# Kernel optimization log

Hardware: AMD Instinct MI355X
Metric: run time of the kernel (lower is better)

Reference implementation:

```python
import jax, jax.numpy as jnp
import numpy as np

B, S, D, DK, DV = 4, 4096, 1024, 64, 64


def setup_inputs() -> dict:
    rng = jax.random.key(0)
    k1, k2, k3, k4, k5, k6 = jax.random.split(rng, 6)
    query = jax.random.normal(k1, (B, S, D), dtype=jnp.float32)
    key = jax.random.normal(k2, (B, S, D), dtype=jnp.float32)
    value = jax.random.normal(k3, (B, S, D), dtype=jnp.float32)
    Wq = jax.random.normal(k4, (D, DK), dtype=jnp.float32)
    Wk = jax.random.normal(k5, (D, DK), dtype=jnp.float32)
    Wv = jax.random.normal(k6, (D, DV), dtype=jnp.float32)
    mask = jnp.tril(jnp.ones((S, S), dtype=jnp.bool_))  # causal mask, broadcasts over batch
    return {"query": query, "key": key, "value": value,
            "Wq": Wq, "Wk": Wk, "Wv": Wv, "mask": mask}


def reference(query, key, value, Wq, Wk, Wv, mask):
    # linear projections: [B,S,D] @ [D,dk] -> [B,S,dk]
    q = jnp.matmul(query, Wq)
    k = jnp.matmul(key, Wk)
    v = jnp.matmul(value, Wv)
    scale = 1.0 / jnp.sqrt(jnp.asarray(DK, dtype=q.dtype))
    # scores: [B,S,S]
    attn = jnp.einsum("bqd,bkd->bqk", q, k) * scale
    attn = jnp.where(mask, attn, -jnp.inf)  # mask==0 -> -inf
    attn = jax.nn.softmax(attn, axis=-1)
    x = jnp.matmul(attn, v)  # [B,S,dv]
    return x
```

## Files before the change

kernel.cpp:

```cpp
#include <hip/hip_runtime.h>
#include <math.h>


#define SEQ 4096
#define DIM 1024
#define HD  64
#define NB  4
#define NSPLIT 4

typedef __attribute__((ext_vector_type(4))) float    f32x4;
typedef __attribute__((ext_vector_type(8))) _Float16 f16x8;
typedef __attribute__((ext_vector_type(4))) _Float16 f16x4;

#define MFMA16 __builtin_amdgcn_mfma_f32_16x16x32_f16

#define GLD16(dst, ptr, imm)                                        \
  asm volatile("global_load_dwordx4 %0, %1, off offset:" #imm      \
               : "=&v"(dst) : "v"(ptr))

#define VMWAIT(n)                                                   \
  do {                                                              \
    asm volatile("s_waitcnt vmcnt(" #n ")" ::: "memory");           \
    __builtin_amdgcn_sched_barrier(0);                              \
  } while (0)

#define LGKMBAR()                                                   \
  do {                                                              \
    asm volatile("s_waitcnt lgkmcnt(0)" ::: "memory");              \
    __builtin_amdgcn_sched_barrier(0);                              \
    asm volatile("s_barrier" ::: "memory");                         \
    __builtin_amdgcn_sched_barrier(0);                              \
  } while (0)

__device__ __forceinline__ int SW(int row, int k) {
  return row * 64 + (k ^ ((row & 7) << 3));
}

__global__ __launch_bounds__(256) void wsplit_kernel(
    const float* __restrict__ Wq, const float* __restrict__ Wk,
    const float* __restrict__ Wv, _Float16* __restrict__ wf)
{
  const int which = blockIdx.x;
  const int kt    = blockIdx.y;
  const float* __restrict__ W = (which == 0) ? Wq : (which == 1) ? Wk : Wv;
  const float scale = (which == 0) ? 0.18033688011112042f : 1.0f;
  const size_t tb = ((size_t)which * 16 + kt) * 8192;
#pragma unroll
  for (int i = 0; i < 2; ++i) {
    const int pair = threadIdx.x + 256 * i;
    const int lane = pair & 63, f = pair >> 6;
    const int ks = f >> 2, ct = f & 3;
    const int col = ct * 16 + (lane & 15);
    const int k0 = kt * 64 + ks * 32 + (lane >> 4) * 8;
    f16x8 hv, lv;
#pragma unroll
    for (int j = 0; j < 8; ++j) {
      const float y = W[(size_t)(k0 + j) * HD + col] * scale;
      const _Float16 h = (_Float16)y;
      hv[j] = h;
      lv[j] = (_Float16)(y - (float)h);
    }
    *(f16x8*)&wf[tb + (size_t)f * 512 + lane * 8]       = hv;
    *(f16x8*)&wf[tb + (size_t)(8 + f) * 512 + lane * 8] = lv;
  }
}

__global__ __launch_bounds__(256, 2) void proj_kernel(
    const float* __restrict__ Xq, const float* __restrict__ Xk,
    const float* __restrict__ Xv,
    const _Float16* __restrict__ wf,
    _Float16* __restrict__ qh, _Float16* __restrict__ ql,
    _Float16* __restrict__ kh, _Float16* __restrict__ kl,
    _Float16* __restrict__ vt)
{
  __shared__ __attribute__((aligned(16))) float    Xs[2][64 * 64];
  __shared__ __attribute__((aligned(16))) _Float16 Ws[2][8192];

  const int which = blockIdx.y;
  const float* __restrict__ X = (which == 0) ? Xq : (which == 1) ? Xk : Xv;

  const int t = threadIdx.x, lane = t & 63, w = t >> 6;
  const int bm = blockIdx.x * 64;

  const float* gX[4];
  int xdst[4];
#pragma unroll
  for (int i = 0; i < 4; ++i) {
    const int row = w * 16 + i * 4 + (lane >> 4);
    gX[i] = X + (size_t)(bm + row) * DIM + (lane & 15) * 4;
    xdst[i] = row * 64 + (((lane & 15) ^ (row & 15)) * 4);
  }
  const _Float16* gW0 = wf + (size_t)which * 131072 + (w * 4) * 512 + lane * 8;
  int wdst[4];
#pragma unroll
  for (int i = 0; i < 4; ++i) wdst[i] = (w * 4 + i) * 512 + lane * 8;

  const int frow = lane & 15;
  const int ldsrow = w * 16 + frow;

  f32x4 acc[4] = {{0,0,0,0},{0,0,0,0},{0,0,0,0},{0,0,0,0}};
  f32x4 xA[4], xB[4];
  f16x8 wA[4], wB[4];

#define LOADT(xs, ws, kt)                                            \
  do {                                                               \
    const float* xb0 = gX[0] + (kt) * 64;                            \
    const float* xb1 = gX[1] + (kt) * 64;                            \
    const float* xb2 = gX[2] + (kt) * 64;                            \
    const float* xb3 = gX[3] + (kt) * 64;                            \
    GLD16(xs[0], xb0, 0);                                            \
    GLD16(xs[1], xb1, 0);                                            \
    GLD16(xs[2], xb2, 0);                                            \
    GLD16(xs[3], xb3, 0);                                            \
    const _Float16* wb = gW0 + (size_t)(kt) * 8192;                  \
    GLD16(ws[0], wb, 0);                                             \
    GLD16(ws[1], wb, 1024);                                          \
    GLD16(ws[2], wb, 2048);                                          \
    GLD16(ws[3], wb, 3072);                                          \
  } while (0)

#define WRITET(xs, ws, buf)                                          \
  do {                                                               \
    _Pragma("unroll")                                                \
    for (int i = 0; i < 4; ++i) *(f32x4*)&Xs[buf][xdst[i]] = xs[i];  \
    _Pragma("unroll")                                                \
    for (int i = 0; i < 4; ++i) *(f16x8*)&Ws[buf][wdst[i]] = ws[i];  \
  } while (0)

#define COMPUTET(buf)                                                     \
  do {                                                                    \
    _Pragma("unroll")                                                     \
    for (int ks = 0; ks < 2; ++ks) {                                      \
      const int cc0 = ks * 8 + (lane >> 4) * 2;                           \
      f32x4 x0 = *(const f32x4*)&Xs[buf][ldsrow * 64 + ((cc0 ^ frow) * 4)];       \
      f32x4 x1 = *(const f32x4*)&Xs[buf][ldsrow * 64 + (((cc0 + 1) ^ frow) * 4)]; \
      f16x8 xh, xl;                                                       \
      _Pragma("unroll")                                                   \
      for (int j = 0; j < 4; ++j) {                                       \
        const _Float16 h0 = (_Float16)x0[j];                              \
        xh[j] = h0; xl[j] = (_Float16)(x0[j] - (float)h0);                \
        const _Float16 h1 = (_Float16)x1[j];                              \
        xh[j + 4] = h1; xl[j + 4] = (_Float16)(x1[j] - (float)h1);        \
      }                                                                   \
      _Pragma("unroll")                                                   \
      for (int ct = 0; ct < 4; ++ct) {                                    \
        f16x8 bh = *(const f16x8*)&Ws[buf][(ks * 4 + ct) * 512 + lane * 8];       \
        f16x8 bl = *(const f16x8*)&Ws[buf][(8 + ks * 4 + ct) * 512 + lane * 8];   \
        acc[ct] = MFMA16(xh, bh, acc[ct], 0, 0, 0);                       \
        acc[ct] = MFMA16(xl, bh, acc[ct], 0, 0, 0);                       \
        acc[ct] = MFMA16(xh, bl, acc[ct], 0, 0, 0);                       \
      }                                                                   \
    }                                                                     \
  } while (0)

  LOADT(xA, wA, 0);
  LOADT(xB, wB, 1);

#pragma unroll 1
  for (int kt = 0; kt < 12; kt += 2) {
    VMWAIT(8);
    WRITET(xA, wA, 0);
    LOADT(xA, wA, kt + 2);
    LGKMBAR();
    COMPUTET(0);
    VMWAIT(8);
    WRITET(xB, wB, 1);
    LOADT(xB, wB, kt + 3);
    LGKMBAR();
    COMPUTET(1);
  }
  VMWAIT(8);  WRITET(xA, wA, 0);  LOADT(xA, wA, 14);  LGKMBAR();  COMPUTET(0);
  VMWAIT(8);  WRITET(xB, wB, 1);  LOADT(xB, wB, 15);  LGKMBAR();  COMPUTET(1);
  VMWAIT(8);  WRITET(xA, wA, 0);                      LGKMBAR();  COMPUTET(0);
  VMWAIT(0);  WRITET(xB, wB, 1);                      LGKMBAR();  COMPUTET(1);
#undef LOADT
#undef WRITET
#undef COMPUTET

  const size_t orow0 = (size_t)bm + w * 16 + (lane >> 4) * 4;
  if (which < 2) {
    _Float16* oh = (which == 0) ? qh : kh;
    _Float16* ol = (which == 0) ? ql : kl;
#pragma unroll
    for (int ct = 0; ct < 4; ++ct)
#pragma unroll
      for (int r = 0; r < 4; ++r) {
        const float y = acc[ct][r];
        const _Float16 h = (_Float16)y;
        const size_t idx = (orow0 + r) * HD + ct * 16 + (lane & 15);
        oh[idx] = h;
        ol[idx] = (_Float16)(y - (float)h);
      }
  } else {
    const int batch = (int)(orow0 >> 12);
    const int pos = (int)(orow0 & 4095);
#pragma unroll
    for (int ct = 0; ct < 4; ++ct) {
      f16x4 hv;
#pragma unroll
      for (int r = 0; r < 4; ++r) hv[r] = (_Float16)acc[ct][r];
      *(f16x4*)&vt[((size_t)batch * HD + ct * 16 + (lane & 15)) * SEQ + pos] = hv;
    }
  }
}

__global__ __launch_bounds__(256) void attn_kernel(
    const _Float16* __restrict__ qh, const _Float16* __restrict__ ql,
    const _Float16* __restrict__ kh, const _Float16* __restrict__ kl,
    const _Float16* __restrict__ vt,
    _Float16* __restrict__ opart, float* __restrict__ mlp)
{
  __shared__ __attribute__((aligned(16))) _Float16 Ksh[64 * 64];
  __shared__ __attribute__((aligned(16))) _Float16 Ksl[64 * 64];
  __shared__ __attribute__((aligned(16))) _Float16 Vs [64 * 64];
  __shared__ __attribute__((aligned(16))) _Float16 Pt [64 * 64];

  const int t = threadIdx.x, lane = t & 63, w = t >> 6;
  const int b = blockIdx.y;
  const int p = blockIdx.x >> 2, s = blockIdx.x & 3;
  const size_t bS = (size_t)b * SEQ;

  for (int sel = 0; sel < 2; ++sel) {
    const int qb = sel ? (63 - p) : p;
    const int qrow0 = qb * 64 + w * 16;
    const int nt = (qb >= s) ? ((qb - s) >> 2) + 1 : 0;

    float m[4] = {-INFINITY, -INFINITY, -INFINITY, -INFINITY};
    float lsum[4] = {0.f, 0.f, 0.f, 0.f};
    f32x4 o[4] = {{0,0,0,0},{0,0,0,0},{0,0,0,0},{0,0,0,0}};

    if (nt > 0) {
      const _Float16* qhp = qh + (bS + qrow0 + (lane & 15)) * HD + ((lane >> 4) * 8);
      const _Float16* qlp = ql + (bS + qrow0 + (lane & 15)) * HD + ((lane >> 4) * 8);
      f16x8 qhf[2], qlf[2];
      qhf[0] = *(const f16x8*)(qhp);      qhf[1] = *(const f16x8*)(qhp + 32);
      qlf[0] = *(const f16x8*)(qlp);      qlf[1] = *(const f16x8*)(qlp + 32);

      for (int i = 0; i < nt; ++i) {
        const int kt = s + 4 * i;
        const int j0 = kt * 64;

        __syncthreads();
#pragma unroll
        for (int c = 0; c < 2; ++c) {
          const int lin = t + 256 * c;
          const int row = lin >> 3, d8 = (lin & 7) * 8;
          const int dst = SW(row, d8);
          *(f16x8*)&Ksh[dst] = *(const f16x8*)&kh[(bS + j0 + row) * HD + d8];
          *(f16x8*)&Ksl[dst] = *(const f16x8*)&kl[(bS + j0 + row) * HD + d8];
          *(f16x8*)&Vs[dst]  = *(const f16x8*)&vt[((size_t)b * HD + row) * SEQ + j0 + d8];
        }
        __syncthreads();

        f32x4 sacc[4] = {{0,0,0,0},{0,0,0,0},{0,0,0,0},{0,0,0,0}};
#pragma unroll
        for (int kk = 0; kk < 2; ++kk)
#pragma unroll
          for (int kt4 = 0; kt4 < 4; ++kt4) {
            const int ba = SW(kt4 * 16 + (lane & 15), kk * 32 + (lane >> 4) * 8);
            f16x8 bh = *(const f16x8*)&Ksh[ba];
            f16x8 bl = *(const f16x8*)&Ksl[ba];
            sacc[kt4] = MFMA16(qhf[kk], bh, sacc[kt4], 0, 0, 0);
            sacc[kt4] = MFMA16(qlf[kk], bh, sacc[kt4], 0, 0, 0);
            sacc[kt4] = MFMA16(qhf[kk], bl, sacc[kt4], 0, 0, 0);
          }

        if (kt == qb) {
#pragma unroll
          for (int kt4 = 0; kt4 < 4; ++kt4) {
            const int key = j0 + kt4 * 16 + (lane & 15);
#pragma unroll
            for (int r = 0; r < 4; ++r)
              if (key > qrow0 + (lane >> 4) * 4 + r) sacc[kt4][r] = -INFINITY;
          }
        }

        float alf[4];
#pragma unroll
        for (int r = 0; r < 4; ++r) {
          float mx = fmaxf(fmaxf(sacc[0][r], sacc[1][r]),
                           fmaxf(sacc[2][r], sacc[3][r]));
          mx = fmaxf(mx, __shfl_xor(mx, 1));
          mx = fmaxf(mx, __shfl_xor(mx, 2));
          mx = fmaxf(mx, __shfl_xor(mx, 4));
          mx = fmaxf(mx, __shfl_xor(mx, 8));
          const float mn = fmaxf(m[r], mx);
          const float al = exp2f(m[r] - mn);
          const int prow = w * 16 + (lane >> 4) * 4 + r;
          float ps = 0.f;
#pragma unroll
          for (int kt4 = 0; kt4 < 4; ++kt4) {
            const _Float16 ph = (_Float16)exp2f(sacc[kt4][r] - mn);
            ps += (float)ph;
            Pt[SW(prow, kt4 * 16 + (lane & 15))] = ph;
          }
          ps += __shfl_xor(ps, 1);
          ps += __shfl_xor(ps, 2);
          ps += __shfl_xor(ps, 4);
          ps += __shfl_xor(ps, 8);
          lsum[r] = lsum[r] * al + ps;
          m[r] = mn;
          alf[r] = al;
        }
        const f32x4 av = {alf[0], alf[1], alf[2], alf[3]};
#pragma unroll
        for (int ct = 0; ct < 4; ++ct) o[ct] *= av;

#pragma unroll
        for (int kk = 0; kk < 2; ++kk) {
          f16x8 pa = *(const f16x8*)&Pt[SW(w * 16 + (lane & 15),
                                           kk * 32 + (lane >> 4) * 8)];
#pragma unroll
          for (int ct = 0; ct < 4; ++ct) {
            f16x8 vb = *(const f16x8*)&Vs[SW(ct * 16 + (lane & 15),
                                             kk * 32 + (lane >> 4) * 8)];
            o[ct] = MFMA16(pa, vb, o[ct], 0, 0, 0);
          }
        }
      }
    }

    f32x4 invv;
#pragma unroll
    for (int r = 0; r < 4; ++r) invv[r] = (nt > 0) ? 1.0f / lsum[r] : 0.0f;
    const size_t ridx0 = (size_t)(b * NSPLIT + s) * SEQ + qrow0 + (lane >> 4) * 4;
#pragma unroll
    for (int ct = 0; ct < 4; ++ct)
#pragma unroll
      for (int r = 0; r < 4; ++r)
        opart[(ridx0 + r) * HD + ct * 16 + (lane & 15)] =
            (_Float16)(o[ct][r] * invv[r]);
    if ((lane & 15) == 0) {
#pragma unroll
      for (int r = 0; r < 4; ++r) {
        mlp[(ridx0 + r) * 2]     = m[r];
        mlp[(ridx0 + r) * 2 + 1] = lsum[r];
      }
    }
  }
}

__global__ __launch_bounds__(256) void combine_kernel(
    const _Float16* __restrict__ opart, const float* __restrict__ mlp,
    float* __restrict__ out)
{
  const int g = blockIdx.x * 256 + threadIdx.x;
  const int row = g >> 4;
  const int cq = (g & 15) * 4;
  const int b = row >> 12, pos = row & 4095;

  float mv[4], lv[4], msx = -INFINITY;
#pragma unroll
  for (int s = 0; s < 4; ++s) {
    const size_t ri = (size_t)(b * NSPLIT + s) * SEQ + pos;
    mv[s] = mlp[ri * 2];
    lv[s] = mlp[ri * 2 + 1];
    msx = fmaxf(msx, mv[s]);
  }
  f32x4 num = {0.f, 0.f, 0.f, 0.f};
  float L = 0.f;
#pragma unroll
  for (int s = 0; s < 4; ++s) {
    const float wgt = lv[s] * exp2f(mv[s] - msx);
    L += wgt;
    const size_t ri = (size_t)(b * NSPLIT + s) * SEQ + pos;
    const f16x4 ov = *(const f16x4*)&opart[ri * HD + cq];
#pragma unroll
    for (int j = 0; j < 4; ++j) num[j] += wgt * (float)ov[j];
  }
  const float inv = 1.0f / L;
  f32x4 res = {num[0] * inv, num[1] * inv, num[2] * inv, num[3] * inv};
  *(f32x4*)&out[(size_t)row * HD + cq] = res;
}

extern "C" void kernel_launch(void* const* d_in, const int* in_sizes, int n_in,
                              void* d_out, int out_size, void* d_ws, size_t ws_size,
                              hipStream_t stream) {
  const float* query = (const float*)d_in[0];
  const float* key   = (const float*)d_in[1];
  const float* value = (const float*)d_in[2];
  const float* Wq    = (const float*)d_in[3];
  const float* Wk    = (const float*)d_in[4];
  const float* Wv    = (const float*)d_in[5];

  float* out = (float*)d_out;

  _Float16* qh  = (_Float16*)d_ws;
  _Float16* ql  = qh  + (size_t)NB * SEQ * HD;
  _Float16* kh  = ql  + (size_t)NB * SEQ * HD;
  _Float16* kl  = kh  + (size_t)NB * SEQ * HD;
  _Float16* vt  = kl  + (size_t)NB * SEQ * HD;
  _Float16* wf  = vt  + (size_t)NB * SEQ * HD;
  _Float16* opart = wf + (size_t)3 * 16 * 8192;
  float* mlp = (float*)(opart + (size_t)NB * NSPLIT * SEQ * HD);

  wsplit_kernel<<<dim3(3, 16), 256, 0, stream>>>(Wq, Wk, Wv, wf);
  proj_kernel<<<dim3(256, 3), 256, 0, stream>>>(query, key, value, wf,
                                                qh, ql, kh, kl, vt);
  attn_kernel<<<dim3(128, NB), 256, 0, stream>>>(qh, ql, kh, kl, vt, opart, mlp);
  combine_kernel<<<1024, 256, 0, stream>>>(opart, mlp, out);
}
```

Before: 94.61 us.

## Load X operand directly into registers, skipping LDS staging in projection kernel

The projection kernel no longer stages the fp32 X tile through shared memory. Each lane now loads the X fragments it needs for MFMA straight from global memory into registers, in batches of four k-tiles, while only the W tiles still go through LDS. This removes the LDS writes and reads for X, the swizzle bookkeeping and half of the shared memory, which may allow more occupancy. The cost is less overlap: the old loop prefetched the next tile while computing the current one, and the new loop waits on each batch of loads with no cross-iteration prefetch. It also holds more registers live, and global accesses per lane become strided rows.

```diff
diff --git a/kernel.cpp b/kernel.cpp
--- a/kernel.cpp
+++ b/kernel.cpp
@@ -73,7 +73,6 @@
     _Float16* __restrict__ kh, _Float16* __restrict__ kl,
     _Float16* __restrict__ vt)
 {
-  __shared__ __attribute__((aligned(16))) float    Xs[2][64 * 64];
   __shared__ __attribute__((aligned(16))) _Float16 Ws[2][8192];
 
   const int which = blockIdx.y;
@@ -82,58 +81,29 @@
   const int t = threadIdx.x, lane = t & 63, w = t >> 6;
   const int bm = blockIdx.x * 64;
 
-  const float* gX[4];
-  int xdst[4];
-#pragma unroll
-  for (int i = 0; i < 4; ++i) {
-    const int row = w * 16 + i * 4 + (lane >> 4);
-    gX[i] = X + (size_t)(bm + row) * DIM + (lane & 15) * 4;
-    xdst[i] = row * 64 + (((lane & 15) ^ (row & 15)) * 4);
-  }
+  const float* xb = X + (size_t)(bm + w * 16 + (lane & 15)) * DIM
+                      + ((lane >> 4) * 8);
   const _Float16* gW0 = wf + (size_t)which * 131072 + (w * 4) * 512 + lane * 8;
   int wdst[4];
 #pragma unroll
   for (int i = 0; i < 4; ++i) wdst[i] = (w * 4 + i) * 512 + lane * 8;
 
-  const int frow = lane & 15;
-  const int ldsrow = w * 16 + frow;
-
   f32x4 acc[4] = {{0,0,0,0},{0,0,0,0},{0,0,0,0},{0,0,0,0}};
-  f32x4 xA[4], xB[4];
-  f16x8 wA[4], wB[4];
-
-#define LOADT(xs, ws, kt)                                            \
-  do {                                                               \
-    const float* xb0 = gX[0] + (kt) * 64;                            \
-    const float* xb1 = gX[1] + (kt) * 64;                            \
-    const float* xb2 = gX[2] + (kt) * 64;                            \
-    const float* xb3 = gX[3] + (kt) * 64;                            \
-    GLD16(xs[0], xb0, 0);                                            \
-    GLD16(xs[1], xb1, 0);                                            \
-    GLD16(xs[2], xb2, 0);                                            \
-    GLD16(xs[3], xb3, 0);                                            \
-    const _Float16* wb = gW0 + (size_t)(kt) * 8192;                  \
-    GLD16(ws[0], wb, 0);                                             \
-    GLD16(ws[1], wb, 1024);                                          \
-    GLD16(ws[2], wb, 2048);                                          \
-    GLD16(ws[3], wb, 3072);                                          \
-  } while (0)
-
-#define WRITET(xs, ws, buf)                                          \
+  f32x4 xr[16];
+  f16x8 wrA[4], wrB[4], wrC[4], wrD[4];
+
+#define WWRITE(wr, buf)                                              \
   do {                                                               \
     _Pragma("unroll")                                                \
-    for (int i = 0; i < 4; ++i) *(f32x4*)&Xs[buf][xdst[i]] = xs[i];  \
-    _Pragma("unroll")                                                \
-    for (int i = 0; i < 4; ++i) *(f16x8*)&Ws[buf][wdst[i]] = ws[i];  \
+    for (int i = 0; i < 4; ++i) *(f16x8*)&Ws[buf][wdst[i]] = wr[i];  \
   } while (0)
 
-#define COMPUTET(buf)                                                     \
+#define COMPT(buf, base)                                                  \
   do {                                                                    \
     _Pragma("unroll")                                                     \
     for (int ks = 0; ks < 2; ++ks) {                                      \
-      const int cc0 = ks * 8 + (lane >> 4) * 2;                           \
-      f32x4 x0 = *(const f32x4*)&Xs[buf][ldsrow * 64 + ((cc0 ^ frow) * 4)];       \
-      f32x4 x1 = *(const f32x4*)&Xs[buf][ldsrow * 64 + (((cc0 + 1) ^ frow) * 4)]; \
+      f32x4 x0 = xr[(base) + 2 * ks];                                     \
+      f32x4 x1 = xr[(base) + 2 * ks + 1];                                 \
       f16x8 xh, xl;                                                       \
       _Pragma("unroll")                                                   \
       for (int j = 0; j < 4; ++j) {                                       \
@@ -153,29 +123,41 @@
     }                                                                     \
   } while (0)
 
-  LOADT(xA, wA, 0);
-  LOADT(xB, wB, 1);
-
 #pragma unroll 1
-  for (int kt = 0; kt < 12; kt += 2) {
+  for (int ss = 0; ss < 4; ++ss) {
+    const float* xs = xb + ss * 256;
+    GLD16(xr[0],  xs, 0);    GLD16(xr[1],  xs, 16);
+    GLD16(xr[2],  xs, 128);  GLD16(xr[3],  xs, 144);
+    GLD16(xr[4],  xs, 256);  GLD16(xr[5],  xs, 272);
+    GLD16(xr[6],  xs, 384);  GLD16(xr[7],  xs, 400);
+    GLD16(xr[8],  xs, 512);  GLD16(xr[9],  xs, 528);
+    GLD16(xr[10], xs, 640);  GLD16(xr[11], xs, 656);
+    GLD16(xr[12], xs, 768);  GLD16(xr[13], xs, 784);
+    GLD16(xr[14], xs, 896);  GLD16(xr[15], xs, 912);
+    const _Float16* wt0 = gW0 + (size_t)(4 * ss) * 8192;
+    const _Float16* wt1 = wt0 + 8192;
+    const _Float16* wt2 = wt0 + 16384;
+    const _Float16* wt3 = wt0 + 24576;
+    GLD16(wrA[0], wt0, 0); GLD16(wrA[1], wt0, 1024);
+    GLD16(wrA[2], wt0, 2048); GLD16(wrA[3], wt0, 3072);
+    GLD16(wrB[0], wt1, 0); GLD16(wrB[1], wt1, 1024);
+    GLD16(wrB[2], wt1, 2048); GLD16(wrB[3], wt1, 3072);
+    GLD16(wrC[0], wt2, 0); GLD16(wrC[1], wt2, 1024);
+    GLD16(wrC[2], wt2, 2048); GLD16(wrC[3], wt2, 3072);
+    GLD16(wrD[0], wt3, 0); GLD16(wrD[1], wt3, 1024);
+    GLD16(wrD[2], wt3, 2048); GLD16(wrD[3], wt3, 3072);
+
+    VMWAIT(12);
+    WWRITE(wrA, 0);  LGKMBAR();  COMPT(0, 0);
     VMWAIT(8);
-    WRITET(xA, wA, 0);
-    LOADT(xA, wA, kt + 2);
-    LGKMBAR();
-    COMPUTET(0);
-    VMWAIT(8);
-    WRITET(xB, wB, 1);
-    LOADT(xB, wB, kt + 3);
-    LGKMBAR();
-    COMPUTET(1);
-  }
-  VMWAIT(8);  WRITET(xA, wA, 0);  LOADT(xA, wA, 14);  LGKMBAR();  COMPUTET(0);
-  VMWAIT(8);  WRITET(xB, wB, 1);  LOADT(xB, wB, 15);  LGKMBAR();  COMPUTET(1);
-  VMWAIT(8);  WRITET(xA, wA, 0);                      LGKMBAR();  COMPUTET(0);
-  VMWAIT(0);  WRITET(xB, wB, 1);                      LGKMBAR();  COMPUTET(1);
-#undef LOADT
-#undef WRITET
-#undef COMPUTET
+    WWRITE(wrB, 1);  LGKMBAR();  COMPT(1, 4);
+    VMWAIT(4);
+    WWRITE(wrC, 0);  LGKMBAR();  COMPT(0, 8);
+    VMWAIT(0);
+    WWRITE(wrD, 1);  LGKMBAR();  COMPT(1, 12);
+  }
+#undef WWRITE
+#undef COMPT
 
   const size_t orow0 = (size_t)bm + w * 16 + (lane >> 4) * 4;
   if (which < 2) {
```

After: 103.2 us. 9.1% more time.

## Load projection X tiles directly into registers and widen blocks to 512 threads

Applied to the files above, without the earlier changes.

The projection kernel no longer stages X through shared memory. Each lane loads its MFMA A-fragment straight from global memory into registers, and only the split-fp16 weights stay double-buffered in LDS. Blocks grow to 512 threads covering 128 rows, the grid halves, and each tile's next load is issued after its compute. This removes the LDS write/read round trip and its swizzle for X, at the cost of less coalesced global X loads (32-byte chunks per row) and a changed latency-hiding schedule.

```diff
diff --git a/kernel.cpp b/kernel.cpp
--- a/kernel.cpp
+++ b/kernel.cpp
@@ -65,7 +65,7 @@
   }
 }
 
-__global__ __launch_bounds__(256, 2) void proj_kernel(
+__global__ __launch_bounds__(512, 4) void proj_kernel(
     const float* __restrict__ Xq, const float* __restrict__ Xk,
     const float* __restrict__ Xv,
     const _Float16* __restrict__ wf,
@@ -73,67 +73,47 @@
     _Float16* __restrict__ kh, _Float16* __restrict__ kl,
     _Float16* __restrict__ vt)
 {
-  __shared__ __attribute__((aligned(16))) float    Xs[2][64 * 64];
   __shared__ __attribute__((aligned(16))) _Float16 Ws[2][8192];
 
   const int which = blockIdx.y;
   const float* __restrict__ X = (which == 0) ? Xq : (which == 1) ? Xk : Xv;
 
   const int t = threadIdx.x, lane = t & 63, w = t >> 6;
-  const int bm = blockIdx.x * 64;
-
-  const float* gX[4];
-  int xdst[4];
-#pragma unroll
-  for (int i = 0; i < 4; ++i) {
-    const int row = w * 16 + i * 4 + (lane >> 4);
-    gX[i] = X + (size_t)(bm + row) * DIM + (lane & 15) * 4;
-    xdst[i] = row * 64 + (((lane & 15) ^ (row & 15)) * 4);
-  }
-  const _Float16* gW0 = wf + (size_t)which * 131072 + (w * 4) * 512 + lane * 8;
-  int wdst[4];
-#pragma unroll
-  for (int i = 0; i < 4; ++i) wdst[i] = (w * 4 + i) * 512 + lane * 8;
-
-  const int frow = lane & 15;
-  const int ldsrow = w * 16 + frow;
+  const int bm = blockIdx.x * 128;
+
+  const float* xb = X + (size_t)(bm + w * 16 + (lane & 15)) * DIM
+                      + ((lane >> 4) * 8);
+  const _Float16* gW = wf + (size_t)which * 131072 + 16 * t;
+  const int wd = 16 * t;
 
   f32x4 acc[4] = {{0,0,0,0},{0,0,0,0},{0,0,0,0},{0,0,0,0}};
   f32x4 xA[4], xB[4];
-  f16x8 wA[4], wB[4];
+  f16x8 wA[2], wB[2];
 
 #define LOADT(xs, ws, kt)                                            \
   do {                                                               \
-    const float* xb0 = gX[0] + (kt) * 64;                            \
-    const float* xb1 = gX[1] + (kt) * 64;                            \
-    const float* xb2 = gX[2] + (kt) * 64;                            \
-    const float* xb3 = gX[3] + (kt) * 64;                            \
-    GLD16(xs[0], xb0, 0);                                            \
-    GLD16(xs[1], xb1, 0);                                            \
-    GLD16(xs[2], xb2, 0);                                            \
-    GLD16(xs[3], xb3, 0);                                            \
-    const _Float16* wb = gW0 + (size_t)(kt) * 8192;                  \
-    GLD16(ws[0], wb, 0);                                             \
-    GLD16(ws[1], wb, 1024);                                          \
-    GLD16(ws[2], wb, 2048);                                          \
-    GLD16(ws[3], wb, 3072);                                          \
-  } while (0)
-
-#define WRITET(xs, ws, buf)                                          \
+    const float* xp = xb + (kt) * 64;                                \
+    GLD16(xs[0], xp, 0);                                             \
+    GLD16(xs[1], xp, 16);                                            \
+    GLD16(xs[2], xp, 128);                                           \
+    GLD16(xs[3], xp, 144);                                           \
+    const _Float16* wp = gW + (size_t)(kt) * 8192;                   \
+    GLD16(ws[0], wp, 0);                                             \
+    GLD16(ws[1], wp, 16);                                            \
+  } while (0)
+
+#define WWRITE(ws, buf)                                              \
   do {                                                               \
-    _Pragma("unroll")                                                \
-    for (int i = 0; i < 4; ++i) *(f32x4*)&Xs[buf][xdst[i]] = xs[i];  \
-    _Pragma("unroll")                                                \
-    for (int i = 0; i < 4; ++i) *(f16x8*)&Ws[buf][wdst[i]] = ws[i];  \
-  } while (0)
-
-#define COMPUTET(buf)                                                     \
+    *(f16x8*)&Ws[buf][wd]     = ws[0];                               \
+    *(f16x8*)&Ws[buf][wd + 8] = ws[1];                               \
+  } while (0)
+
+#define COMPUTET(xs, buf)                                                 \
   do {                                                                    \
     _Pragma("unroll")                                                     \
     for (int ks = 0; ks < 2; ++ks) {                                      \
-      const int cc0 = ks * 8 + (lane >> 4) * 2;                           \
-      f32x4 x0 = *(const f32x4*)&Xs[buf][ldsrow * 64 + ((cc0 ^ frow) * 4)];       \
-      f32x4 x1 = *(const f32x4*)&Xs[buf][ldsrow * 64 + (((cc0 + 1) ^ frow) * 4)]; \
+      f32x4 x0 = xs[2 * ks];                                              \
+      f32x4 x1 = xs[2 * ks + 1];                                          \
       f16x8 xh, xl;                                                       \
       _Pragma("unroll")                                                   \
       for (int j = 0; j < 4; ++j) {                                       \
@@ -158,23 +138,23 @@
 
 #pragma unroll 1
   for (int kt = 0; kt < 12; kt += 2) {
-    VMWAIT(8);
-    WRITET(xA, wA, 0);
+    VMWAIT(6);
+    WWRITE(wA, 0);
+    LGKMBAR();
+    COMPUTET(xA, 0);
     LOADT(xA, wA, kt + 2);
+    VMWAIT(6);
+    WWRITE(wB, 1);
     LGKMBAR();
-    COMPUTET(0);
-    VMWAIT(8);
-    WRITET(xB, wB, 1);
+    COMPUTET(xB, 1);
     LOADT(xB, wB, kt + 3);
-    LGKMBAR();
-    COMPUTET(1);
-  }
-  VMWAIT(8);  WRITET(xA, wA, 0);  LOADT(xA, wA, 14);  LGKMBAR();  COMPUTET(0);
-  VMWAIT(8);  WRITET(xB, wB, 1);  LOADT(xB, wB, 15);  LGKMBAR();  COMPUTET(1);
-  VMWAIT(8);  WRITET(xA, wA, 0);                      LGKMBAR();  COMPUTET(0);
-  VMWAIT(0);  WRITET(xB, wB, 1);                      LGKMBAR();  COMPUTET(1);
+  }
+  VMWAIT(6);  WWRITE(wA, 0);  LGKMBAR();  COMPUTET(xA, 0);  LOADT(xA, wA, 14);
+  VMWAIT(6);  WWRITE(wB, 1);  LGKMBAR();  COMPUTET(xB, 1);  LOADT(xB, wB, 15);
+  VMWAIT(6);  WWRITE(wA, 0);  LGKMBAR();  COMPUTET(xA, 0);
+  VMWAIT(0);  WWRITE(wB, 1);  LGKMBAR();  COMPUTET(xB, 1);
 #undef LOADT
-#undef WRITET
+#undef WWRITE
 #undef COMPUTET
 
   const size_t orow0 = (size_t)bm + w * 16 + (lane >> 4) * 4;
@@ -395,7 +375,7 @@
   float* mlp = (float*)(opart + (size_t)NB * NSPLIT * SEQ * HD);
 
   wsplit_kernel<<<dim3(3, 16), 256, 0, stream>>>(Wq, Wk, Wv, wf);
-  proj_kernel<<<dim3(256, 3), 256, 0, stream>>>(query, key, value, wf,
+  proj_kernel<<<dim3(128, 3), 512, 0, stream>>>(query, key, value, wf,
                                                 qh, ql, kh, kl, vt);
   attn_kernel<<<dim3(128, NB), 256, 0, stream>>>(qh, ql, kh, kl, vt, opart, mlp);
   combine_kernel<<<1024, 256, 0, stream>>>(opart, mlp, out);
```

After: 97.44 us. 3.0% more time.
